# Optimization experiments

Measured on AMD Instinct MI355X. Metric: run time of the kernel, lower is better.

The kernel has to match this reference:

```python
import jax, jax.numpy as jnp
import numpy as np

B, T, C, A, D, H, W = 2, 16, 64, 64, 32, 32, 32  # batch, timepoints, channels, att_features, spatial


def setup_inputs() -> dict:
    key = jax.random.key(0)
    ks = jax.random.split(key, 7)
    s = 1.0 / np.sqrt(C)
    return {
        "x": jax.random.normal(ks[0], (B, T, C, D, H, W), dtype=jnp.float32),
        "Wk": jax.random.normal(ks[1], (A, C), dtype=jnp.float32) * s,
        "bk": jax.random.normal(ks[2], (A,), dtype=jnp.float32) * s,
        "Wq": jax.random.normal(ks[3], (A, C), dtype=jnp.float32) * s,
        "bq": jax.random.normal(ks[4], (A,), dtype=jnp.float32) * s,
        "Wv": jax.random.normal(ks[5], (C, C), dtype=jnp.float32) * s,
        "bv": jax.random.normal(ks[6], (C,), dtype=jnp.float32) * s,
    }


def reference(x, Wk, bk, Wq, bq, Wv, bv):
    # kernel=1 Conv3d == pointwise channel mixing. Project and move spatial
    # dims to the front exactly like movedim((3,4,5),(1,2,3)):
    # result layout [B, D, H, W, T, out_ch].
    def proj(Wt, bt):
        return jnp.einsum('btcdhw,oc->bdhwto', x, Wt) + bt

    k = proj(Wk, bk)  # [B,D,H,W,T,A]
    q = proj(Wq, bq)  # [B,D,H,W,T,A]
    v = proj(Wv, bv)  # [B,D,H,W,T,C]

    scale = 1.0 / np.sqrt(float(Wk.shape[0]))  # sqrt(att_features)
    att = jnp.einsum('bdhwta,bdhwsa->bdhwts', k, q) * scale  # [B,D,H,W,T,T]
    # norm = partial(softmax, dim=1) on the 6-D tensor -> softmax over spatial D axis
    att_map = jax.nn.softmax(att, axis=1)

    # features = (value^T @ att_map)^T: feat[...,s,c] = sum_t v[...,t,c] * att_map[...,t,s]
    feat = jnp.einsum('bdhwtc,bdhwts->bdhwsc', v, att_map)  # [B,D,H,W,T,C]
    # movedim((1,2,3),(3,4,5)): back to [B, T, C, D, H, W]
    return jnp.transpose(feat, (0, 4, 5, 1, 2, 3))
```

## Files before the change

### kernel.cpp

```cpp
#include <hip/hip_runtime.h>

typedef short v8s __attribute__((ext_vector_type(8)));
typedef float v4f __attribute__((ext_vector_type(4)));
typedef float v2f __attribute__((ext_vector_type(2)));

#define NSP 32768
#define XSTR 2056
#define WS_ZP_B 65536ull

__device__ __forceinline__ unsigned short f2bf(float f) {
  union { float f; unsigned u; } v; v.f = f;
  unsigned r = v.u + 0x7fffu + ((v.u >> 16) & 1u);
  return (unsigned short)(r >> 16);
}
__device__ __forceinline__ unsigned pk(float a, float b) {
  return (unsigned)f2bf(a) | ((unsigned)f2bf(b) << 16);
}

union UF8 { v8s v; unsigned u[4]; uint4 q; };


__global__ __launch_bounds__(512) void prep_kernel(
    const float* __restrict__ Wk, const float* __restrict__ bk,
    const float* __restrict__ Wq, const float* __restrict__ bq,
    const float* __restrict__ Wv, unsigned* __restrict__ ws) {
  __shared__ float sWk[4096], sWq[4096], sWv[4096], sbk[64], sbq[64];
  for (int i = threadIdx.x; i < 4096; i += 512) { sWk[i] = Wk[i]; sWq[i] = Wq[i]; sWv[i] = Wv[i]; }
  if (threadIdx.x < 64) { sbk[threadIdx.x] = bk[threadIdx.x]; sbq[threadIdx.x] = bq[threadIdx.x]; }
  __syncthreads();
  for (int task = threadIdx.x; task < 18 * 64; task += 512) {
    int f = task >> 6, lane = task & 63;
    int i16 = lane & 15, g = lane >> 4;
    unsigned short e[8];
    #pragma unroll
    for (int j = 0; j < 8; ++j) {
      int k = (((j >> 2) << 4) + 4 * g + (j & 3));
      float acc = 0.f;
      if (f < 8) {
        int row = ((f >> 1) << 4) + i16;
        int cc  = ((f & 1) << 5) + k;
        for (int a = 0; a < 64; ++a) acc += sWk[a * 64 + row] * sWq[a * 64 + cc];
      } else if (f < 10) {
        int c = ((f - 8) << 5) + k;
        if (i16 == 0)      { for (int a = 0; a < 64; ++a) acc += sWk[a * 64 + c] * sbq[a]; }
        else if (i16 == 1) { for (int a = 0; a < 64; ++a) acc += sbk[a] * sWq[a * 64 + c]; }
      } else {
        int c  = (((f - 10) >> 1) << 4) + i16;
        int cp = (((f - 10) & 1) << 5) + k;
        acc = sWv[c * 64 + cp];
      }
      e[j] = f2bf(acc);
    }
    unsigned* dst = ws + (size_t)(f * 64 + lane) * 4;
    dst[0] = e[0] | ((unsigned)e[1] << 16);
    dst[1] = e[2] | ((unsigned)e[3] << 16);
    dst[2] = e[4] | ((unsigned)e[5] << 16);
    dst[3] = e[6] | ((unsigned)e[7] << 16);
  }
  if (threadIdx.x == 0) {
    float beta = 0.f;
    for (int a = 0; a < 64; ++a) beta += sbk[a] * sbq[a];
    ((float*)ws)[18 * 256] = beta;
  }
}

#define S2L 0.18033688011112042f

#define DECODE512() \
  int bid = (int)blockIdx.x; \
  int b = bid & 1, dcc = (bid >> 1) & 7, h = bid >> 4; \
  const int d0 = dcc << 2; \
  const size_t base0 = (size_t)b * 33554432 + h * 32;

#define STAGE_DEFS(BUF) \
  const int w2 = tid & 15; \
  const int rp0 = tid >> 4; \
  v2f sA[8], sB[8]; \
  auto issueH = [&](int d, int half) { \
    const float* xp = x + base0 + (size_t)d * 1024; \
    _Pragma("unroll") \
    for (int i = 0; i < 8; ++i) { \
      int rp = half * 256 + (i << 5) + rp0; \
      const float* r0 = xp + (size_t)(2 * rp) * NSP + 2 * w2; \
      sA[i] = *(const v2f*)r0; \
      sB[i] = *(const v2f*)(r0 + NSP); \
    } \
  }; \
  auto writeH = [&](int half) { \
    _Pragma("unroll") \
    for (int i = 0; i < 8; ++i) { \
      int rp = half * 256 + (i << 5) + rp0; \
      int t = rp >> 5, c = (rp & 31) << 1; \
      int off = (t << 7) + (((c << 1)) ^ ((t & 7) << 4)); \
      *(unsigned*)(&BUF[(2 * w2) * XSTR + off])     = pk(sA[i].x, sB[i].x); \
      *(unsigned*)(&BUF[(2 * w2 + 1) * XSTR + off]) = pk(sA[i].y, sB[i].y); \
    } \
  };

#define LOADX_DEF(BUF) \
  auto loadX = [&](int loc, v8s fX[2]) { \
    const unsigned char* bp = &BUF[loc * XSTR + (i16 << 7)]; \
    const int sw = (i16 & 7) << 4; \
    _Pragma("unroll") \
    for (int kc = 0; kc < 2; ++kc) { \
      union { v8s v; unsigned long long dd[2]; } u; \
      int o = (kc << 6) + (g << 3); \
      u.dd[0] = *(const unsigned long long*)(bp + (o ^ sw)); \
      u.dd[1] = *(const unsigned long long*)(bp + ((o + 32) ^ sw)); \
      fX[kc] = u.v; \
    } \
  };

#define LDF_DEF() \
  auto ldf = [&](int f) -> v8s { \
    union { v8s v; uint4 q; } u; \
    u.q = *(const uint4*)&Wm[(f << 8) + (lane << 2)]; \
    return u.v; \
  };

#define ATTOF_DEF() \
  auto attOf = [&](const v8s fX[2]) -> v4f { \
    v4f accW[4]; \
    _Pragma("unroll") \
    for (int tr = 0; tr < 4; ++tr) { \
      v8s m0 = ldf(2 * tr), m1 = ldf(2 * tr + 1); \
      v4f a = {0.f, 0.f, 0.f, 0.f}; \
      a = __builtin_amdgcn_mfma_f32_16x16x32_bf16(m0, fX[0], a, 0, 0, 0); \
      a = __builtin_amdgcn_mfma_f32_16x16x32_bf16(m1, fX[1], a, 0, 0, 0); \
      accW[tr] = a; \
    } \
    v8s u0 = ldf(8), u1 = ldf(9); \
    v4f au = {0.f, 0.f, 0.f, 0.f}; \
    au = __builtin_amdgcn_mfma_f32_16x16x32_bf16(u0, fX[0], au, 0, 0, 0); \
    au = __builtin_amdgcn_mfma_f32_16x16x32_bf16(u1, fX[1], au, 0, 0, 0); \
    float a1v = au[0] + beta; \
    float a2v = au[1]; \
    float a2s = __shfl(a2v, i16); \
    v4f att; \
    _Pragma("unroll") \
    for (int j = 0; j < 4; ++j) att[j] = __shfl(a1v, 4 * g + j) + a2s; \
    _Pragma("unroll") \
    for (int kc = 0; kc < 2; ++kc) { \
      UF8 w; \
      w.u[0] = pk(accW[2 * kc][0], accW[2 * kc][1]); \
      w.u[1] = pk(accW[2 * kc][2], accW[2 * kc][3]); \
      w.u[2] = pk(accW[2 * kc + 1][0], accW[2 * kc + 1][1]); \
      w.u[3] = pk(accW[2 * kc + 1][2], accW[2 * kc + 1][3]); \
      att = __builtin_amdgcn_mfma_f32_16x16x32_bf16(fX[kc], w.v, att, 0, 0, 0); \
    } \
    return att; \
  };

#define FEATQ(tn, FB) do { \
  _Pragma("unroll") \
  for (int l = 0; l < 4; ++l) { \
    int wq = 4 * wv + l; \
    UF8 fP; fP.u[0] = Pp[l][0]; fP.u[1] = Pp[l][1]; fP.u[2] = 0; fP.u[3] = 0; \
    UF8 fV; fV.u[0] = vp[l][2 * (tn)]; fV.u[1] = vp[l][2 * (tn) + 1]; fV.u[2] = 0; fV.u[3] = 0; \
    v4f ft = {0.f, 0.f, 0.f, 0.f}; \
    ft = __builtin_amdgcn_mfma_f32_16x16x32_bf16(fP.v, fV.v, ft, 0, 0, 0); \
    _Pragma("unroll") \
    for (int j = 0; j < 4; ++j) { \
      int r = (4 * g + j) * 16 + i16; \
      (FB)[r * 33 + (wq ^ g)] = ft[j]; \
    } \
  } \
} while (0)

__global__ __launch_bounds__(512) void pass1_z(
    const float* __restrict__ x, const unsigned* __restrict__ ws,
    float* __restrict__ zp) {
  __shared__ __align__(16) unsigned char Xbuf[32 * XSTR];
  __shared__ unsigned Wm[2560];

  const int tid = (int)threadIdx.x;
  const int lane = tid & 63, wv = tid >> 6;
  const int i16 = lane & 15, g = lane >> 4;
  DECODE512();

  for (int o = tid; o < 2560; o += 512) Wm[o] = ws[o];
  const float beta = ((const float*)ws)[4608];

  STAGE_DEFS(Xbuf);
  LOADX_DEF(Xbuf);
  LDF_DEF();
  ATTOF_DEF();

  float Z[4][4] = {};
  issueH(d0, 0);
  for (int ii = 0; ii < 4; ++ii) {
    const int d = d0 + ii;
    __syncthreads();
    writeH(0);
    issueH(d, 1);
    writeH(1);
    __syncthreads();
    if (ii < 3) issueH(d + 1, 0);
    #pragma unroll
    for (int l = 0; l < 4; ++l) {
      v8s fX[2]; loadX(4 * wv + l, fX);
      v4f att = attOf(fX);
      #pragma unroll
      for (int j = 0; j < 4; ++j) Z[l][j] += exp2f(att[j] * S2L);
    }
  }
  const int locg = b * 1024 + h * 32 + 4 * wv;
  #pragma unroll
  for (int l = 0; l < 4; ++l)
    #pragma unroll
    for (int j = 0; j < 4; ++j)
      zp[(((size_t)dcc * 2048 + locg + l) << 8) + (4 * g + j) * 16 + i16] = Z[l][j];
}

__global__ __launch_bounds__(512) void pass2_out(
    const float* __restrict__ x, const float* __restrict__ bv,
    const unsigned* __restrict__ ws, const float* __restrict__ zp,
    float* __restrict__ out) {
  __shared__ __align__(16) unsigned char UNI[67584];
  __shared__ unsigned Wm[2560];

  const int tid = (int)threadIdx.x;
  const int lane = tid & 63, wv = tid >> 6;
  const int i16 = lane & 15, g = lane >> 4;
  DECODE512();

  for (int o = tid; o < 2560; o += 512) Wm[o] = ws[o];
  const float beta = ((const float*)ws)[4608];
  float bvv[4];
  #pragma unroll
  for (int tn = 0; tn < 4; ++tn) bvv[tn] = bv[i16 + 16 * tn];

  float iZ[4][4];
  #pragma unroll
  for (int l = 0; l < 4; ++l) {
    const int locg = b * 1024 + h * 32 + 4 * wv + l;
    #pragma unroll
    for (int j = 0; j < 4; ++j) {
      float s = 0.f;
      #pragma unroll
      for (int c2 = 0; c2 < 8; ++c2)
        s += zp[(((size_t)c2 * 2048 + locg) << 8) + (4 * g + j) * 16 + i16];
      iZ[l][j] = 1.f / s;
    }
  }

  STAGE_DEFS(UNI);
  LOADX_DEF(UNI);
  LDF_DEF();
  ATTOF_DEF();

  float* FbA = (float*)UNI;
  float* FbB = FbA + 8448;
  const uint4* W4 = (const uint4*)ws;

  auto storeQ = [&](int tn, int d, const float* FB) {
    float* op = out + base0 + (size_t)d * 1024 + (size_t)(16 * tn) * NSP;
    const int w4 = tid & 7, rr = tid >> 3;
    #pragma unroll
    for (int it = 0; it < 4; ++it) {
      int r = (it << 6) + rr;
      const float* fp = &FB[r * 33 + (w4 << 2)];
      float4 val;
      val.x = fp[0 ^ it]; val.y = fp[1 ^ it]; val.z = fp[2 ^ it]; val.w = fp[3 ^ it];
      *(float4*)(op + (size_t)((r >> 4) * 64 + (r & 15)) * NSP + (w4 << 2)) = val;
    }
  };

  issueH(d0, 0);
  for (int ii = 0; ii < 4; ++ii) {
    const int d = d0 + ii;
    __syncthreads();
    writeH(0);
    issueH(d, 1);
    writeH(1);
    __syncthreads();
    if (ii < 3) issueH(d + 1, 0);

    unsigned Pp[4][2], vp[4][8];
    #pragma unroll
    for (int l = 0; l < 4; ++l) {
      v8s fX[2]; loadX(4 * wv + l, fX);
      v4f att = attOf(fX);
      float p0 = exp2f(att[0] * S2L) * iZ[l][0];
      float p1 = exp2f(att[1] * S2L) * iZ[l][1];
      float p2 = exp2f(att[2] * S2L) * iZ[l][2];
      float p3 = exp2f(att[3] * S2L) * iZ[l][3];
      Pp[l][0] = pk(p0, p1); Pp[l][1] = pk(p2, p3);
      #pragma unroll
      for (int tn = 0; tn < 4; ++tn) {
        UF8 wa, wb;
        wa.q = W4[(10 + 2 * tn) * 64 + lane];
        wb.q = W4[(11 + 2 * tn) * 64 + lane];
        v4f a = {bvv[tn], bvv[tn], bvv[tn], bvv[tn]};
        a = __builtin_amdgcn_mfma_f32_16x16x32_bf16(fX[0], wa.v, a, 0, 0, 0);
        a = __builtin_amdgcn_mfma_f32_16x16x32_bf16(fX[1], wb.v, a, 0, 0, 0);
        vp[l][2 * tn] = pk(a[0], a[1]); vp[l][2 * tn + 1] = pk(a[2], a[3]);
      }
    }
    __syncthreads();

    FEATQ(0, FbA);
    __syncthreads();
    storeQ(0, d, FbA); FEATQ(1, FbB);
    __syncthreads();
    storeQ(1, d, FbB); FEATQ(2, FbA);
    __syncthreads();
    storeQ(2, d, FbA); FEATQ(3, FbB);
    __syncthreads();
    storeQ(3, d, FbB);
  }
}

extern "C" void kernel_launch(void* const* d_in, const int* in_sizes, int n_in,
                              void* d_out, int out_size, void* d_ws, size_t ws_size,
                              hipStream_t stream) {
  const float* x  = (const float*)d_in[0];
  const float* Wk = (const float*)d_in[1];
  const float* bk = (const float*)d_in[2];
  const float* Wq = (const float*)d_in[3];
  const float* bq = (const float*)d_in[4];
  const float* Wv = (const float*)d_in[5];
  const float* bv = (const float*)d_in[6];
  float* out = (float*)d_out;
  unsigned* ws = (unsigned*)d_ws;
  float* zp = (float*)((char*)d_ws + WS_ZP_B);

  prep_kernel<<<1, 512, 0, stream>>>(Wk, bk, Wq, bq, Wv, ws);
  pass1_z<<<512, 512, 0, stream>>>(x, ws, zp);
  pass2_out<<<512, 512, 0, stream>>>(x, bv, ws, zp, out);
}
```

Before: 298.0 us.

## Halve pass1 grid with 8-depth chunks and prefetch full next slab during compute

pass1 now runs 256 blocks, each covering 8 depth slices instead of 4, so only 4 partial Z sums are produced and pass2 reduces 4 partials instead of 8. Both passes now hold both halves of the staging registers, and the next slice's global loads are issued interleaved with compute (between attention groups in pass1, between FEATQ/store phases in pass2) rather than in a serialized write/issue/write sequence. The aim is to hide global load latency behind MFMA and store work, at the cost of higher register pressure (double staging arrays) and fewer blocks in pass1, which may lower occupancy.

```diff
diff --git a/kernel.cpp b/kernel.cpp
--- a/kernel.cpp
+++ b/kernel.cpp
@@ -66,6 +66,12 @@
 
 #define S2L 0.18033688011112042f
 
+#define DECODE256() \
+  int bid = (int)blockIdx.x; \
+  int b = bid & 1, dc = (bid >> 1) & 3, h = bid >> 3; \
+  const int d0 = dc << 3; \
+  const size_t base0 = (size_t)b * 33554432 + h * 32;
+
 #define DECODE512() \
   int bid = (int)blockIdx.x; \
   int b = bid & 1, dcc = (bid >> 1) & 7, h = bid >> 4; \
@@ -75,15 +81,15 @@
 #define STAGE_DEFS(BUF) \
   const int w2 = tid & 15; \
   const int rp0 = tid >> 4; \
-  v2f sA[8], sB[8]; \
+  v2f sA[16], sB[16]; \
   auto issueH = [&](int d, int half) { \
     const float* xp = x + base0 + (size_t)d * 1024; \
     _Pragma("unroll") \
     for (int i = 0; i < 8; ++i) { \
       int rp = half * 256 + (i << 5) + rp0; \
       const float* r0 = xp + (size_t)(2 * rp) * NSP + 2 * w2; \
-      sA[i] = *(const v2f*)r0; \
-      sB[i] = *(const v2f*)(r0 + NSP); \
+      sA[half * 8 + i] = *(const v2f*)r0; \
+      sB[half * 8 + i] = *(const v2f*)(r0 + NSP); \
     } \
   }; \
   auto writeH = [&](int half) { \
@@ -92,8 +98,8 @@
       int rp = half * 256 + (i << 5) + rp0; \
       int t = rp >> 5, c = (rp & 31) << 1; \
       int off = (t << 7) + (((c << 1)) ^ ((t & 7) << 4)); \
-      *(unsigned*)(&BUF[(2 * w2) * XSTR + off])     = pk(sA[i].x, sB[i].x); \
-      *(unsigned*)(&BUF[(2 * w2 + 1) * XSTR + off]) = pk(sA[i].y, sB[i].y); \
+      *(unsigned*)(&BUF[(2 * w2) * XSTR + off])     = pk(sA[half * 8 + i].x, sB[half * 8 + i].x); \
+      *(unsigned*)(&BUF[(2 * w2 + 1) * XSTR + off]) = pk(sA[half * 8 + i].y, sB[half * 8 + i].y); \
     } \
   };
 
@@ -176,7 +182,7 @@
   const int tid = (int)threadIdx.x;
   const int lane = tid & 63, wv = tid >> 6;
   const int i16 = lane & 15, g = lane >> 4;
-  DECODE512();
+  DECODE256();
 
   for (int o = tid; o < 2560; o += 512) Wm[o] = ws[o];
   const float beta = ((const float*)ws)[4608];
@@ -187,29 +193,35 @@
   ATTOF_DEF();
 
   float Z[4][4] = {};
-  issueH(d0, 0);
-  for (int ii = 0; ii < 4; ++ii) {
+  issueH(d0, 0); issueH(d0, 1);
+  for (int ii = 0; ii < 8; ++ii) {
     const int d = d0 + ii;
     __syncthreads();
-    writeH(0);
-    issueH(d, 1);
-    writeH(1);
-    __syncthreads();
-    if (ii < 3) issueH(d + 1, 0);
-    #pragma unroll
-    for (int l = 0; l < 4; ++l) {
+    writeH(0); writeH(1);
+    __syncthreads();
+    if (ii < 7) issueH(d + 1, 0);
+    #pragma unroll
+    for (int l = 0; l < 2; ++l) {
       v8s fX[2]; loadX(4 * wv + l, fX);
       v4f att = attOf(fX);
       #pragma unroll
       for (int j = 0; j < 4; ++j) Z[l][j] += exp2f(att[j] * S2L);
     }
+    if (ii < 7) issueH(d + 1, 1);
+    #pragma unroll
+    for (int l = 2; l < 4; ++l) {
+      v8s fX[2]; loadX(4 * wv + l, fX);
+      v4f att = attOf(fX);
+      #pragma unroll
+      for (int j = 0; j < 4; ++j) Z[l][j] += exp2f(att[j] * S2L);
+    }
   }
   const int locg = b * 1024 + h * 32 + 4 * wv;
   #pragma unroll
   for (int l = 0; l < 4; ++l)
     #pragma unroll
     for (int j = 0; j < 4; ++j)
-      zp[(((size_t)dcc * 2048 + locg + l) << 8) + (4 * g + j) * 16 + i16] = Z[l][j];
+      zp[(((size_t)dc * 2048 + locg + l) << 8) + (4 * g + j) * 16 + i16] = Z[l][j];
 }
 
 __global__ __launch_bounds__(512) void pass2_out(
@@ -238,7 +250,7 @@
     for (int j = 0; j < 4; ++j) {
       float s = 0.f;
       #pragma unroll
-      for (int c2 = 0; c2 < 8; ++c2)
+      for (int c2 = 0; c2 < 4; ++c2)
         s += zp[(((size_t)c2 * 2048 + locg) << 8) + (4 * g + j) * 16 + i16];
       iZ[l][j] = 1.f / s;
     }
@@ -266,15 +278,12 @@
     }
   };
 
-  issueH(d0, 0);
+  issueH(d0, 0); issueH(d0, 1);
   for (int ii = 0; ii < 4; ++ii) {
     const int d = d0 + ii;
     __syncthreads();
-    writeH(0);
-    issueH(d, 1);
-    writeH(1);
-    __syncthreads();
-    if (ii < 3) issueH(d + 1, 0);
+    writeH(0); writeH(1);
+    __syncthreads();
 
     unsigned Pp[4][2], vp[4][8];
     #pragma unroll
@@ -301,11 +310,15 @@
 
     FEATQ(0, FbA);
     __syncthreads();
-    storeQ(0, d, FbA); FEATQ(1, FbB);
+    storeQ(0, d, FbA);
+    if (ii < 3) issueH(d + 1, 0);
+    FEATQ(1, FbB);
     __syncthreads();
     storeQ(1, d, FbB); FEATQ(2, FbA);
     __syncthreads();
-    storeQ(2, d, FbA); FEATQ(3, FbB);
+    storeQ(2, d, FbA);
+    if (ii < 3) issueH(d + 1, 1);
+    FEATQ(3, FbB);
     __syncthreads();
     storeQ(3, d, FbB);
   }
@@ -326,6 +339,6 @@
   float* zp = (float*)((char*)d_ws + WS_ZP_B);
 
   prep_kernel<<<1, 512, 0, stream>>>(Wk, bk, Wq, bq, Wv, ws);
-  pass1_z<<<512, 512, 0, stream>>>(x, ws, zp);
+  pass1_z<<<256, 512, 0, stream>>>(x, ws, zp);
   pass2_out<<<512, 512, 0, stream>>>(x, bv, ws, zp, out);
 }
```

Result: slower. 304.9 us (+2.3%).
